# Optimization experiments

Measured on AMD Instinct MI355X. Metric: run time of the kernel, lower is better.

## Reference

```python
import jax, jax.numpy as jnp
import numpy as np
from jax import lax

# init_kwargs constants
DO_TUBE = False
TAU = 0.3
ITERATIONS = 5
BLEND_FACTOR = 0.3


def _avg_pool3(x):
    """3x3x3 avg pool, stride 1, zero padding 1, count_include_pad=True.
    x: (n, h, w, d). Matches torch F.avg_pool3d(kernel=3, stride=1, padding=1)."""
    s = lax.reduce_window(x, 0.0, lax.add, (1, 3, 3, 3), (1, 1, 1, 1), 'SAME')
    return s * (1.0 / 27.0)


def setup_inputs() -> dict:
    key = jax.random.key(0)
    # binary mask (b, 1, h, w, d) as docstring requires
    u = jax.random.uniform(key, (2, 1, 256, 256, 256), dtype=jnp.float32)
    seg = (u > 0.5).astype(jnp.float32)
    return {"segmentation": seg}


def reference(segmentation):
    b, c, h, w, d = segmentation.shape
    x = segmentation.reshape(b * c, h, w, d)

    # NOTE: in the original code `mask` is never updated inside the iteration
    # loop, so every iteration adds the identical term; the loop over the
    # batch dim is also trivially batchable. Compute the per-iteration term
    # once (fully batched) and scale by ITERATIONS.
    eroded = -_avg_pool3(-x)            # differentiable erosion
    dilated = _avg_pool3(eroded)        # differentiable dilation
    diff = x - dilated
    term = jax.nn.sigmoid((diff - 0.5) / TAU) + diff  # soft_threshold + residual
    skeleton = ITERATIONS * term

    skeleton = skeleton.reshape(b, c, h, w, d)
    # DO_TUBE is False (the torch code path for True is broken for 5D input)
    skeleton = BLEND_FACTOR * segmentation + (1.0 - BLEND_FACTOR) * skeleton
    skeleton = jnp.round(jnp.clip(skeleton, 0.0, 1.0))
    return 1.0 - skeleton
```

## Files before the change

### kernel.cpp

```cpp
#include <hip/hip_runtime.h>
#include <stdint.h>


#define SLABS 512
#define CH 32
#define NCHUNK 8
#define WAVES (SLABS * NCHUNK)
#define BLOCKS (WAVES / 4)

__device__ __forceinline__ uint32_t row_pack(const float4 v, const int ln) {
    uint32_t b = (v.x > 0.5f ? 0x1u : 0u)
               | (v.y > 0.5f ? 0x100u : 0u)
               | (v.z > 0.5f ? 0x10000u : 0u)
               | (v.w > 0.5f ? 0x1000000u : 0u);
    uint32_t up = (uint32_t)__shfl_up((int)b, 1);
    uint32_t dn = (uint32_t)__shfl_down((int)b, 1);
    if (ln == 0)  up = 0u;
    if (ln == 63) dn = 0u;
    uint64_t W = (uint64_t)(up >> 16) | ((uint64_t)b << 16)
               | ((uint64_t)(dn & 0xffffu) << 48);
    uint64_t S = W + ((W >> 8) << 1) + (W >> 16) * 3u + ((W >> 24) << 1) + (W >> 32);
    uint32_t n = (uint32_t)S;
    if (ln == 0)  n -= (b & 0xffu);
    if (ln == 63) n -= (b & 0xff000000u);
    return n | (b << 7);
}

__global__ __launch_bounds__(256) void skel_k1(const float* __restrict__ x,
                                               uint32_t* __restrict__ ws) {
    const int ln    = threadIdx.x & 63;
    const int wid   = (blockIdx.x << 2) | (threadIdx.x >> 6);
    const int chunk = wid & (NCHUNK - 1);
    const int slab  = wid >> 3;
    const int w0    = chunk * CH;
    const float4* xs = (const float4*)(x + (size_t)slab * 65536);
    uint32_t* os = ws + (size_t)slab * 16384;

    auto loadrow = [&](int wi) -> uint32_t {
        if (wi < 0 || wi > 255) return 0u;
        return row_pack(xs[wi * 64 + ln], ln);
    };
    uint32_t r0 = loadrow(w0 - 2), r1 = loadrow(w0 - 1), r2 = loadrow(w0),
             r3 = loadrow(w0 + 1), r4 = loadrow(w0 + 2);
    for (int w = w0; w < w0 + CH; ++w) {
        uint32_t rn = loadrow(w + 3);
        uint32_t n0 = r0 & 0x7f7f7f7fu, n1 = r1 & 0x7f7f7f7fu, n2 = r2 & 0x7f7f7f7fu,
                 n3 = r3 & 0x7f7f7f7fu, n4 = r4 & 0x7f7f7f7fu;
        uint32_t s = n0 + (n1 << 1) + n2 * 3u + (n3 << 1) + n4;
        if (w == 0 || w == 255) s -= n2;
        s |= (r2 & 0x80808080u);
        os[w * 64 + ln] = s;
        r0 = r1; r1 = r2; r2 = r3; r3 = r4; r4 = rn;
    }
}

__device__ __forceinline__ float skel_pointwise(uint32_t n, uint32_t xi) {
    float xf   = (float)xi;
    float d    = (float)n * (1.0f / 729.0f);
    float diff = xf - d;
    float t    = (diff - 0.5f) * (1.0f / 0.3f);
    float sg   = 1.0f / (1.0f + expf(-t));
    float v    = 0.3f * xf + 3.5f * (sg + diff);
    v = fminf(fmaxf(v, 0.0f), 1.0f);
    return 1.0f - rintf(v);
}

__global__ __launch_bounds__(256) void skel_k2(const uint32_t* __restrict__ ws,
                                               float4* __restrict__ out) {
    const int ln    = threadIdx.x & 63;
    const int wid   = (blockIdx.x << 2) | (threadIdx.x >> 6);
    const int chunk = wid & (NCHUNK - 1);
    const int col   = wid >> 3;
    const int wi    = col & 255, bi = col >> 8;
    const int h0    = chunk * CH;
    const uint32_t base = (uint32_t)bi * (1u << 22) + (uint32_t)wi * 64u + (uint32_t)ln;

    auto loadrow = [&](int hi) -> uint32_t {
        if (hi < 0 || hi > 255) return 0u;
        return ws[base + (uint32_t)hi * 16384u];
    };
    uint32_t q0 = loadrow(h0 - 2), q1 = loadrow(h0 - 1), q2 = loadrow(h0),
             q3 = loadrow(h0 + 1), q4 = loadrow(h0 + 2);
    for (int h = h0; h < h0 + CH; ++h) {
        uint32_t qn = loadrow(h + 3);
        uint32_t m0 = q0 & 0x7f7f7f7fu, m1 = q1 & 0x7f7f7f7fu, m2 = q2 & 0x7f7f7f7fu,
                 m3 = q3 & 0x7f7f7f7fu, m4 = q4 & 0x7f7f7f7fu;
        uint32_t e0 = m0 & 0x00ff00ffu, e1 = m1 & 0x00ff00ffu, e2 = m2 & 0x00ff00ffu,
                 e3 = m3 & 0x00ff00ffu, e4 = m4 & 0x00ff00ffu;
        uint32_t o0 = (m0 >> 8) & 0x00ff00ffu, o1 = (m1 >> 8) & 0x00ff00ffu,
                 o2 = (m2 >> 8) & 0x00ff00ffu, o3 = (m3 >> 8) & 0x00ff00ffu,
                 o4 = (m4 >> 8) & 0x00ff00ffu;
        uint32_t ae = e0 + (e1 << 1) + e2 * 3u + (e3 << 1) + e4;
        uint32_t ao = o0 + (o1 << 1) + o2 * 3u + (o3 << 1) + o4;
        if (h == 0 || h == 255) { ae -= e2; ao -= o2; }
        const uint32_t xb = q2;
        float4 o;
        o.x = skel_pointwise(ae & 0xffffu, (xb >> 7)  & 1u);
        o.y = skel_pointwise(ao & 0xffffu, (xb >> 15) & 1u);
        o.z = skel_pointwise(ae >> 16,     (xb >> 23) & 1u);
        o.w = skel_pointwise(ao >> 16,     (xb >> 31) & 1u);
        out[base + (uint32_t)h * 16384u] = o;
        q0 = q1; q1 = q2; q2 = q3; q3 = q4; q4 = qn;
    }
}

extern "C" void kernel_launch(void* const* d_in, const int* in_sizes, int n_in,
                              void* d_out, int out_size, void* d_ws, size_t ws_size,
                              hipStream_t stream) {
    const float* x = (const float*)d_in[0];
    uint32_t* ws = (uint32_t*)d_ws;
    skel_k1<<<BLOCKS, 256, 0, stream>>>(x, ws);
    skel_k2<<<BLOCKS, 256, 0, stream>>>(ws, (float4*)d_out);
}
```

Measured before the change: 273.6 us.

## Prefetch rows in groups, use nontemporal I/O, replace sigmoid with integer threshold

Both kernels now clamp row indices so loads are unconditional, and they prefetch four rows ahead in unrolled groups to raise memory-level parallelism. Input loads and output stores use nontemporal hints to avoid polluting the cache. The expf-based pointwise function is replaced by an exact integer comparison (count >= 9 and x == 0), derived because x is binary. This removes transcendental math, though it relies on the input being a binary mask, which the task guarantees.

```diff
diff --git a/kernel.cpp b/kernel.cpp
--- a/kernel.cpp
+++ b/kernel.cpp
@@ -2,17 +2,13 @@
 #include <stdint.h>
 
 
-#define SLABS 512
+typedef float  vfloat4 __attribute__((ext_vector_type(4)));
+
 #define CH 32
 #define NCHUNK 8
-#define WAVES (SLABS * NCHUNK)
-#define BLOCKS (WAVES / 4)
+#define BLOCKS 1024
 
-__device__ __forceinline__ uint32_t row_pack(const float4 v, const int ln) {
-    uint32_t b = (v.x > 0.5f ? 0x1u : 0u)
-               | (v.y > 0.5f ? 0x100u : 0u)
-               | (v.z > 0.5f ? 0x10000u : 0u)
-               | (v.w > 0.5f ? 0x1000000u : 0u);
+__device__ __forceinline__ uint32_t row_pack(uint32_t b, const int ln) {
     uint32_t up = (uint32_t)__shfl_up((int)b, 1);
     uint32_t dn = (uint32_t)__shfl_down((int)b, 1);
     if (ln == 0)  up = 0u;
@@ -26,6 +22,11 @@
     return n | (b << 7);
 }
 
+__device__ __forceinline__ uint32_t bits_of(const vfloat4 v) {
+    return (v.x > 0.5f ? 0x1u : 0u) | (v.y > 0.5f ? 0x100u : 0u)
+         | (v.z > 0.5f ? 0x10000u : 0u) | (v.w > 0.5f ? 0x1000000u : 0u);
+}
+
 __global__ __launch_bounds__(256) void skel_k1(const float* __restrict__ x,
                                                uint32_t* __restrict__ ws) {
     const int ln    = threadIdx.x & 63;
@@ -33,40 +34,51 @@
     const int chunk = wid & (NCHUNK - 1);
     const int slab  = wid >> 3;
     const int w0    = chunk * CH;
-    const float4* xs = (const float4*)(x + (size_t)slab * 65536);
+    const vfloat4* xs = (const vfloat4*)(x + (size_t)slab * 65536);
     uint32_t* os = ws + (size_t)slab * 16384;
 
-    auto loadrow = [&](int wi) -> uint32_t {
-        if (wi < 0 || wi > 255) return 0u;
-        return row_pack(xs[wi * 64 + ln], ln);
+    auto ldraw = [&](int wi) -> vfloat4 {
+        int wc = wi < 0 ? 0 : (wi > 255 ? 255 : wi);
+        return __builtin_nontemporal_load(&xs[wc * 64 + ln]);
     };
-    uint32_t r0 = loadrow(w0 - 2), r1 = loadrow(w0 - 1), r2 = loadrow(w0),
-             r3 = loadrow(w0 + 1), r4 = loadrow(w0 + 2);
-    for (int w = w0; w < w0 + CH; ++w) {
-        uint32_t rn = loadrow(w + 3);
-        uint32_t n0 = r0 & 0x7f7f7f7fu, n1 = r1 & 0x7f7f7f7fu, n2 = r2 & 0x7f7f7f7fu,
-                 n3 = r3 & 0x7f7f7f7fu, n4 = r4 & 0x7f7f7f7fu;
-        uint32_t s = n0 + (n1 << 1) + n2 * 3u + (n3 << 1) + n4;
-        if (w == 0 || w == 255) s -= n2;
-        s |= (r2 & 0x80808080u);
-        os[w * 64 + ln] = s;
-        r0 = r1; r1 = r2; r2 = r3; r3 = r4; r4 = rn;
+    auto packb = [&](vfloat4 v, int wi) -> uint32_t {
+        uint32_t b = bits_of(v);
+        return (wi >= 0 && wi < 256) ? b : 0u;
+    };
+
+    vfloat4 a0 = ldraw(w0 - 2), a1 = ldraw(w0 - 1), a2 = ldraw(w0),
+            a3 = ldraw(w0 + 1), a4 = ldraw(w0 + 2);
+    vfloat4 raw0 = ldraw(w0 + 3), raw1 = ldraw(w0 + 4),
+            raw2 = ldraw(w0 + 5), raw3 = ldraw(w0 + 6);
+    uint32_t r0 = row_pack(packb(a0, w0 - 2), ln);
+    uint32_t r1 = row_pack(packb(a1, w0 - 1), ln);
+    uint32_t r2 = row_pack(packb(a2, w0    ), ln);
+    uint32_t r3 = row_pack(packb(a3, w0 + 1), ln);
+    uint32_t r4 = row_pack(packb(a4, w0 + 2), ln);
+
+    for (int g = 0; g < CH; g += 4) {
+        vfloat4 n0 = ldraw(w0 + g + 7),  n1 = ldraw(w0 + g + 8),
+                n2 = ldraw(w0 + g + 9),  n3 = ldraw(w0 + g + 10);
+        vfloat4 cur[4] = {raw0, raw1, raw2, raw3};
+        #pragma unroll
+        for (int j = 0; j < 4; ++j) {
+            const int w = w0 + g + j;
+            uint32_t rn = row_pack(packb(cur[j], w + 3), ln);
+            uint32_t m0 = r0 & 0x7f7f7f7fu, m1 = r1 & 0x7f7f7f7fu,
+                     m2 = r2 & 0x7f7f7f7fu, m3 = r3 & 0x7f7f7f7fu,
+                     m4 = r4 & 0x7f7f7f7fu;
+            uint32_t s = m0 + (m1 << 1) + m2 * 3u + (m3 << 1) + m4;
+            if (w == 0 || w == 255) s -= m2;
+            s |= (r2 & 0x80808080u);
+            os[w * 64 + ln] = s;
+            r0 = r1; r1 = r2; r2 = r3; r3 = r4; r4 = rn;
+        }
+        raw0 = n0; raw1 = n1; raw2 = n2; raw3 = n3;
     }
 }
 
-__device__ __forceinline__ float skel_pointwise(uint32_t n, uint32_t xi) {
-    float xf   = (float)xi;
-    float d    = (float)n * (1.0f / 729.0f);
-    float diff = xf - d;
-    float t    = (diff - 0.5f) * (1.0f / 0.3f);
-    float sg   = 1.0f / (1.0f + expf(-t));
-    float v    = 0.3f * xf + 3.5f * (sg + diff);
-    v = fminf(fmaxf(v, 0.0f), 1.0f);
-    return 1.0f - rintf(v);
-}
-
 __global__ __launch_bounds__(256) void skel_k2(const uint32_t* __restrict__ ws,
-                                               float4* __restrict__ out) {
+                                               vfloat4* __restrict__ out) {
     const int ln    = threadIdx.x & 63;
     const int wid   = (blockIdx.x << 2) | (threadIdx.x >> 6);
     const int chunk = wid & (NCHUNK - 1);
@@ -75,32 +87,48 @@
     const int h0    = chunk * CH;
     const uint32_t base = (uint32_t)bi * (1u << 22) + (uint32_t)wi * 64u + (uint32_t)ln;
 
-    auto loadrow = [&](int hi) -> uint32_t {
-        if (hi < 0 || hi > 255) return 0u;
-        return ws[base + (uint32_t)hi * 16384u];
+    auto ld = [&](int hi) -> uint32_t {
+        int hc = hi < 0 ? 0 : (hi > 255 ? 255 : hi);
+        return ws[base + (uint32_t)hc * 16384u];
     };
-    uint32_t q0 = loadrow(h0 - 2), q1 = loadrow(h0 - 1), q2 = loadrow(h0),
-             q3 = loadrow(h0 + 1), q4 = loadrow(h0 + 2);
-    for (int h = h0; h < h0 + CH; ++h) {
-        uint32_t qn = loadrow(h + 3);
-        uint32_t m0 = q0 & 0x7f7f7f7fu, m1 = q1 & 0x7f7f7f7fu, m2 = q2 & 0x7f7f7f7fu,
-                 m3 = q3 & 0x7f7f7f7fu, m4 = q4 & 0x7f7f7f7fu;
-        uint32_t e0 = m0 & 0x00ff00ffu, e1 = m1 & 0x00ff00ffu, e2 = m2 & 0x00ff00ffu,
-                 e3 = m3 & 0x00ff00ffu, e4 = m4 & 0x00ff00ffu;
-        uint32_t o0 = (m0 >> 8) & 0x00ff00ffu, o1 = (m1 >> 8) & 0x00ff00ffu,
-                 o2 = (m2 >> 8) & 0x00ff00ffu, o3 = (m3 >> 8) & 0x00ff00ffu,
-                 o4 = (m4 >> 8) & 0x00ff00ffu;
-        uint32_t ae = e0 + (e1 << 1) + e2 * 3u + (e3 << 1) + e4;
-        uint32_t ao = o0 + (o1 << 1) + o2 * 3u + (o3 << 1) + o4;
-        if (h == 0 || h == 255) { ae -= e2; ao -= o2; }
-        const uint32_t xb = q2;
-        float4 o;
-        o.x = skel_pointwise(ae & 0xffffu, (xb >> 7)  & 1u);
-        o.y = skel_pointwise(ao & 0xffffu, (xb >> 15) & 1u);
-        o.z = skel_pointwise(ae >> 16,     (xb >> 23) & 1u);
-        o.w = skel_pointwise(ao >> 16,     (xb >> 31) & 1u);
-        out[base + (uint32_t)h * 16384u] = o;
-        q0 = q1; q1 = q2; q2 = q3; q3 = q4; q4 = qn;
+    auto msk = [&](uint32_t q, int hi) -> uint32_t {
+        return (hi >= 0 && hi < 256) ? q : 0u;
+    };
+
+    uint32_t q0 = msk(ld(h0 - 2), h0 - 2), q1 = msk(ld(h0 - 1), h0 - 1),
+             q2 = ld(h0), q3 = ld(h0 + 1), q4 = ld(h0 + 2);
+    uint32_t p0 = ld(h0 + 3), p1 = ld(h0 + 4), p2 = ld(h0 + 5), p3 = ld(h0 + 6);
+
+    for (int g = 0; g < CH; g += 4) {
+        uint32_t f0 = ld(h0 + g + 7),  f1 = ld(h0 + g + 8),
+                 f2 = ld(h0 + g + 9),  f3 = ld(h0 + g + 10);
+        uint32_t cur[4] = {p0, p1, p2, p3};
+        #pragma unroll
+        for (int j = 0; j < 4; ++j) {
+            const int h = h0 + g + j;
+            uint32_t qn = msk(cur[j], h + 3);
+            uint32_t m0 = q0 & 0x7f7f7f7fu, m1 = q1 & 0x7f7f7f7fu,
+                     m2 = q2 & 0x7f7f7f7fu, m3 = q3 & 0x7f7f7f7fu,
+                     m4 = q4 & 0x7f7f7f7fu;
+            uint32_t e0 = m0 & 0x00ff00ffu, e1 = m1 & 0x00ff00ffu,
+                     e2 = m2 & 0x00ff00ffu, e3 = m3 & 0x00ff00ffu,
+                     e4 = m4 & 0x00ff00ffu;
+            uint32_t o0 = (m0 >> 8) & 0x00ff00ffu, o1 = (m1 >> 8) & 0x00ff00ffu,
+                     o2 = (m2 >> 8) & 0x00ff00ffu, o3 = (m3 >> 8) & 0x00ff00ffu,
+                     o4 = (m4 >> 8) & 0x00ff00ffu;
+            uint32_t ae = e0 + (e1 << 1) + e2 * 3u + (e3 << 1) + e4;
+            uint32_t ao = o0 + (o1 << 1) + o2 * 3u + (o3 << 1) + o4;
+            if (h == 0 || h == 255) { ae -= e2; ao -= o2; }
+            const uint32_t xb = q2;
+            vfloat4 o;
+            o.x = ((ae & 0xffffu) >= 9u && !((xb >> 7)  & 1u)) ? 1.0f : 0.0f;
+            o.y = ((ao & 0xffffu) >= 9u && !((xb >> 15) & 1u)) ? 1.0f : 0.0f;
+            o.z = ((ae >> 16)     >= 9u && !((xb >> 23) & 1u)) ? 1.0f : 0.0f;
+            o.w = ((ao >> 16)     >= 9u && !((xb >> 31) & 1u)) ? 1.0f : 0.0f;
+            __builtin_nontemporal_store(o, &out[base + (uint32_t)h * 16384u]);
+            q0 = q1; q1 = q2; q2 = q3; q3 = q4; q4 = qn;
+        }
+        p0 = f0; p1 = f1; p2 = f2; p3 = f3;
     }
 }
 
@@ -110,5 +138,5 @@
     const float* x = (const float*)d_in[0];
     uint32_t* ws = (uint32_t*)d_ws;
     skel_k1<<<BLOCKS, 256, 0, stream>>>(x, ws);
-    skel_k2<<<BLOCKS, 256, 0, stream>>>(ws, (float4*)d_out);
+    skel_k2<<<BLOCKS, 256, 0, stream>>>(ws, (vfloat4*)d_out);
 }
```

Result: faster. 232.3 us (-15.1%).

## Fuse two-pass packed stencil into single kernel reading fp32 rows with h-streaming

Applied to the files above, without the earlier changes.

Replaces the two kernels, which communicated through a packed uint32 workspace, with one fused kernel. Each wave streams along h, loads five neighbouring w-rows of fp32 input per h, sums them in floats, packs the result and shuffles across lanes for the d direction. The sigmoid pointwise step is replaced by an exact integer threshold test (count >= 9 and x == 0). Stores are nontemporal and blocks are remapped. This removes the workspace write and re-read and the expf calls, but each input row is now read about five times across neighbouring waves, which relies on the cache to absorb it.

```diff
diff --git a/kernel.cpp b/kernel.cpp
--- a/kernel.cpp
+++ b/kernel.cpp
@@ -2,105 +2,108 @@
 #include <stdint.h>
 
 
-#define SLABS 512
-#define CH 32
-#define NCHUNK 8
-#define WAVES (SLABS * NCHUNK)
-#define BLOCKS (WAVES / 4)
+typedef float        vfloat4 __attribute__((ext_vector_type(4)));
+typedef unsigned int vuint4  __attribute__((ext_vector_type(4)));
 
-__device__ __forceinline__ uint32_t row_pack(const float4 v, const int ln) {
-    uint32_t b = (v.x > 0.5f ? 0x1u : 0u)
-               | (v.y > 0.5f ? 0x100u : 0u)
-               | (v.z > 0.5f ? 0x10000u : 0u)
-               | (v.w > 0.5f ? 0x1000000u : 0u);
-    uint32_t up = (uint32_t)__shfl_up((int)b, 1);
-    uint32_t dn = (uint32_t)__shfl_down((int)b, 1);
-    if (ln == 0)  up = 0u;
-    if (ln == 63) dn = 0u;
-    uint64_t W = (uint64_t)(up >> 16) | ((uint64_t)b << 16)
-               | ((uint64_t)(dn & 0xffffu) << 48);
-    uint64_t S = W + ((W >> 8) << 1) + (W >> 16) * 3u + ((W >> 24) << 1) + (W >> 32);
-    uint32_t n = (uint32_t)S;
-    if (ln == 0)  n -= (b & 0xffu);
-    if (ln == 63) n -= (b & 0xff000000u);
-    return n | (b << 7);
-}
+#define CH2 32
+#define BLOCKS 1024
 
-__global__ __launch_bounds__(256) void skel_k1(const float* __restrict__ x,
-                                               uint32_t* __restrict__ ws) {
-    const int ln    = threadIdx.x & 63;
-    const int wid   = (blockIdx.x << 2) | (threadIdx.x >> 6);
-    const int chunk = wid & (NCHUNK - 1);
-    const int slab  = wid >> 3;
-    const int w0    = chunk * CH;
-    const float4* xs = (const float4*)(x + (size_t)slab * 65536);
-    uint32_t* os = ws + (size_t)slab * 16384;
+__global__ __launch_bounds__(256) void skel_fused(const float* __restrict__ x,
+                                                  float* __restrict__ outp) {
+    const int ln  = threadIdx.x & 63;
+    const int wv  = threadIdx.x >> 6;
+    const int bid = blockIdx.x;
+    const int L      = (bid & 7) * 128 + (bid >> 3);
+    const int wblock = L >> 4;
+    const int combo  = L & 15;
+    const int b      = combo & 1;
+    const int hc     = combo >> 1;
+    const int w      = wblock * 4 + wv;
+    const int h0     = hc * CH2;
+    const int hlast  = (h0 + CH2 + 1 > 255) ? 255 : (h0 + CH2 + 1);
 
-    auto loadrow = [&](int wi) -> uint32_t {
-        if (wi < 0 || wi > 255) return 0u;
-        return row_pack(xs[wi * 64 + ln], ln);
+    const vfloat4* __restrict__ xs = (const vfloat4*)x;
+    vfloat4* __restrict__ os = (vfloat4*)outp;
+    const uint32_t rbase = (uint32_t)b * 4194304u + (uint32_t)w * 64u + (uint32_t)ln;
+    const vfloat4 vzero = {0.0f, 0.0f, 0.0f, 0.0f};
+
+    int  co[5]; bool cv[5];
+    #pragma unroll
+    for (int j = 0; j < 5; ++j) {
+        int wj = w + j - 2;
+        cv[j]  = (wj >= 0) && (wj <= 255);
+        int wc = wj < 0 ? 0 : (wj > 255 ? 255 : wj);
+        co[j]  = (wc - w) * 64;
+    }
+
+    auto load5 = [&](int hp, vfloat4 R[5]) {
+        int hcl = hp < 0 ? 0 : (hp > hlast ? hlast : hp);
+        uint32_t rb = rbase + (uint32_t)hcl * 16384u;
+        #pragma unroll
+        for (int j = 0; j < 5; ++j) {
+            vfloat4 v = xs[(int)rb + co[j]];
+            R[j] = cv[j] ? v : vzero;
+        }
     };
-    uint32_t r0 = loadrow(w0 - 2), r1 = loadrow(w0 - 1), r2 = loadrow(w0),
-             r3 = loadrow(w0 + 1), r4 = loadrow(w0 + 2);
-    for (int w = w0; w < w0 + CH; ++w) {
-        uint32_t rn = loadrow(w + 3);
-        uint32_t n0 = r0 & 0x7f7f7f7fu, n1 = r1 & 0x7f7f7f7fu, n2 = r2 & 0x7f7f7f7fu,
-                 n3 = r3 & 0x7f7f7f7fu, n4 = r4 & 0x7f7f7f7fu;
-        uint32_t s = n0 + (n1 << 1) + n2 * 3u + (n3 << 1) + n4;
-        if (w == 0 || w == 255) s -= n2;
-        s |= (r2 & 0x80808080u);
-        os[w * 64 + ln] = s;
-        r0 = r1; r1 = r2; r2 = r3; r3 = r4; r4 = rn;
-    }
-}
 
-__device__ __forceinline__ float skel_pointwise(uint32_t n, uint32_t xi) {
-    float xf   = (float)xi;
-    float d    = (float)n * (1.0f / 729.0f);
-    float diff = xf - d;
-    float t    = (diff - 0.5f) * (1.0f / 0.3f);
-    float sg   = 1.0f / (1.0f + expf(-t));
-    float v    = 0.3f * xf + 3.5f * (sg + diff);
-    v = fminf(fmaxf(v, 0.0f), 1.0f);
-    return 1.0f - rintf(v);
-}
+    auto dw_from = [&](const vfloat4 R[5], int hp) -> uint32_t {
+        if (hp < 0 || hp > 255) return 0u;
+        vfloat4 s = R[0] + R[4] + 2.0f * (R[1] + R[3]) + 3.0f * R[2];
+        if (w == 0 || w == 255) s = s - R[2];
+        uint32_t tn = (uint32_t)s.x | ((uint32_t)s.y << 8)
+                    | ((uint32_t)s.z << 16) | ((uint32_t)s.w << 24);
+        vuint4 u2 = __builtin_bit_cast(vuint4, R[2]);
+        uint32_t tx = ((u2.x >> 22) & 0x80u)   | ((u2.y >> 14) & 0x8000u)
+                    | ((u2.z >> 6) & 0x800000u) | ((u2.w << 2) & 0x80000000u);
+        uint32_t up = (uint32_t)__shfl_up((int)tn, 1);
+        uint32_t dn = (uint32_t)__shfl_down((int)tn, 1);
+        if (ln == 0)  up = 0u;
+        if (ln == 63) dn = 0u;
+        uint64_t W = (uint64_t)(up >> 16) | ((uint64_t)tn << 16)
+                   | ((uint64_t)(dn & 0xffffu) << 48);
+        uint64_t S = W + ((W >> 8) << 1) + (W >> 16) * 3u + ((W >> 24) << 1) + (W >> 32);
+        uint32_t n = (uint32_t)S;
+        if (ln == 0)  n -= (tn & 0xffu);
+        if (ln == 63) n -= (tn & 0xff000000u);
+        return n | tx;
+    };
 
-__global__ __launch_bounds__(256) void skel_k2(const uint32_t* __restrict__ ws,
-                                               float4* __restrict__ out) {
-    const int ln    = threadIdx.x & 63;
-    const int wid   = (blockIdx.x << 2) | (threadIdx.x >> 6);
-    const int chunk = wid & (NCHUNK - 1);
-    const int col   = wid >> 3;
-    const int wi    = col & 255, bi = col >> 8;
-    const int h0    = chunk * CH;
-    const uint32_t base = (uint32_t)bi * (1u << 22) + (uint32_t)wi * 64u + (uint32_t)ln;
-
-    auto loadrow = [&](int hi) -> uint32_t {
-        if (hi < 0 || hi > 255) return 0u;
-        return ws[base + (uint32_t)hi * 16384u];
-    };
-    uint32_t q0 = loadrow(h0 - 2), q1 = loadrow(h0 - 1), q2 = loadrow(h0),
-             q3 = loadrow(h0 + 1), q4 = loadrow(h0 + 2);
-    for (int h = h0; h < h0 + CH; ++h) {
-        uint32_t qn = loadrow(h + 3);
-        uint32_t m0 = q0 & 0x7f7f7f7fu, m1 = q1 & 0x7f7f7f7fu, m2 = q2 & 0x7f7f7f7fu,
-                 m3 = q3 & 0x7f7f7f7fu, m4 = q4 & 0x7f7f7f7fu;
+    auto emit = [&](int h, uint32_t a0, uint32_t a1, uint32_t a2,
+                    uint32_t a3, uint32_t a4) {
+        uint32_t m0 = a0 & 0x7f7f7f7fu, m1 = a1 & 0x7f7f7f7fu, m2 = a2 & 0x7f7f7f7fu,
+                 m3 = a3 & 0x7f7f7f7fu, m4 = a4 & 0x7f7f7f7fu;
         uint32_t e0 = m0 & 0x00ff00ffu, e1 = m1 & 0x00ff00ffu, e2 = m2 & 0x00ff00ffu,
                  e3 = m3 & 0x00ff00ffu, e4 = m4 & 0x00ff00ffu;
         uint32_t o0 = (m0 >> 8) & 0x00ff00ffu, o1 = (m1 >> 8) & 0x00ff00ffu,
                  o2 = (m2 >> 8) & 0x00ff00ffu, o3 = (m3 >> 8) & 0x00ff00ffu,
                  o4 = (m4 >> 8) & 0x00ff00ffu;
-        uint32_t ae = e0 + (e1 << 1) + e2 * 3u + (e3 << 1) + e4;
-        uint32_t ao = o0 + (o1 << 1) + o2 * 3u + (o3 << 1) + o4;
+        uint32_t ae = e0 + e4 + ((e1 + e3) << 1) + e2 * 3u;
+        uint32_t ao = o0 + o4 + ((o1 + o3) << 1) + o2 * 3u;
         if (h == 0 || h == 255) { ae -= e2; ao -= o2; }
-        const uint32_t xb = q2;
-        float4 o;
-        o.x = skel_pointwise(ae & 0xffffu, (xb >> 7)  & 1u);
-        o.y = skel_pointwise(ao & 0xffffu, (xb >> 15) & 1u);
-        o.z = skel_pointwise(ae >> 16,     (xb >> 23) & 1u);
-        o.w = skel_pointwise(ao >> 16,     (xb >> 31) & 1u);
-        out[base + (uint32_t)h * 16384u] = o;
-        q0 = q1; q1 = q2; q2 = q3; q3 = q4; q4 = qn;
+        vfloat4 o;
+        o.x = (((ae & 0xffffu) >= 9u) && !(a2 & 0x80u))       ? 1.0f : 0.0f;
+        o.y = (((ao & 0xffffu) >= 9u) && !(a2 & 0x8000u))     ? 1.0f : 0.0f;
+        o.z = (((ae >> 16) >= 9u)     && !(a2 & 0x800000u))   ? 1.0f : 0.0f;
+        o.w = (((ao >> 16) >= 9u)     && !(a2 & 0x80000000u)) ? 1.0f : 0.0f;
+        __builtin_nontemporal_store(o, &os[rbase + (uint32_t)h * 16384u]);
+    };
+
+    vfloat4 Ra[5], Rb[5], T[5];
+    uint32_t d0, d1, d2, d3, d4, d5;
+    load5(h0 - 2, T); d0 = dw_from(T, h0 - 2);
+    load5(h0 - 1, T); d1 = dw_from(T, h0 - 1);
+    load5(h0,     T); d2 = dw_from(T, h0);
+    load5(h0 + 1, T); d3 = dw_from(T, h0 + 1);
+    load5(h0 + 2, Ra);
+
+    for (int h = h0; h < h0 + CH2; h += 2) {
+        load5(h + 3, Rb);
+        d4 = dw_from(Ra, h + 2);
+        emit(h, d0, d1, d2, d3, d4);
+        load5(h + 4, Ra);
+        d5 = dw_from(Rb, h + 3);
+        emit(h + 1, d1, d2, d3, d4, d5);
+        d0 = d2; d1 = d3; d2 = d4; d3 = d5;
     }
 }
 
@@ -108,7 +111,5 @@
                               void* d_out, int out_size, void* d_ws, size_t ws_size,
                               hipStream_t stream) {
     const float* x = (const float*)d_in[0];
-    uint32_t* ws = (uint32_t*)d_ws;
-    skel_k1<<<BLOCKS, 256, 0, stream>>>(x, ws);
-    skel_k2<<<BLOCKS, 256, 0, stream>>>(ws, (float4*)d_out);
+    skel_fused<<<BLOCKS, 256, 0, stream>>>(x, (float*)d_out);
 }
```

New measurement: 275.4 us. No clear change (+0.7%).
